# Kernel optimization log

Measured on AMD Instinct MI355X. Metric: run time of the kernel, lower is better.

## Reference

```python
import jax, jax.numpy as jnp
import numpy as np

N, E, D, H, C, ED = 100000, 1600000, 128, 8, 16, 16  # nodes, edges, dim, heads, out_ch, edge_dim
NEG_SLOPE = 0.2
LN_EPS = 1e-5


def setup_inputs() -> dict:
    key = jax.random.key(0)
    ks = jax.random.split(key, 16)
    g = 1.0 / np.sqrt(D)
    return {
        "x": jax.random.normal(ks[0], (N, D), jnp.float32),
        "edge_index": jax.random.randint(ks[1], (2, E), 0, N, dtype=jnp.int64),
        "edge_attr": jax.random.normal(ks[2], (E, ED), jnp.float32),
        "lin_W": jax.random.normal(ks[3], (D, H * C), jnp.float32) * g,
        "att_src": jax.random.normal(ks[4], (1, H, C), jnp.float32) * g,
        "att_dst": jax.random.normal(ks[5], (1, H, C), jnp.float32) * g,
        "lin_edge_W": jax.random.normal(ks[6], (ED, H * C), jnp.float32) * (1.0 / np.sqrt(ED)),
        "att_edge": jax.random.normal(ks[7], (1, H, C), jnp.float32) * g,
        "conv_bias": jnp.zeros((H * C,), jnp.float32),
        "ln1_g": jnp.ones((D,), jnp.float32),
        "ln1_b": jnp.zeros((D,), jnp.float32),
        "W1": jax.random.normal(ks[8], (D, D), jnp.float32) * g,
        "b1": jnp.zeros((D,), jnp.float32),
        "W2": jax.random.normal(ks[9], (D, D), jnp.float32) * g,
        "b2": jnp.zeros((D,), jnp.float32),
        "ln2_g": jnp.ones((D,), jnp.float32),
        "ln2_b": jnp.zeros((D,), jnp.float32),
    }


def _layernorm(v, g, b):
    mu = jnp.mean(v, axis=-1, keepdims=True)
    var = jnp.mean(jnp.square(v - mu), axis=-1, keepdims=True)
    return (v - mu) * jax.lax.rsqrt(var + LN_EPS) * g + b


def reference(x, edge_index, edge_attr, lin_W, att_src, att_dst, lin_edge_W,
              att_edge, conv_bias, ln1_g, ln1_b, W1, b1, W2, b2, ln2_g, ln2_b):
    src, dst = edge_index[0], edge_index[1]
    xh = (x @ lin_W).reshape(N, H, C)              # [N,H,C]
    a_src = jnp.sum(xh * att_src, axis=-1)         # [N,H]
    a_dst = jnp.sum(xh * att_dst, axis=-1)         # [N,H]
    e = (edge_attr @ lin_edge_W).reshape(E, H, C)  # [E,H,C]
    alpha = a_src[src] + a_dst[dst] + jnp.sum(e * att_edge, axis=-1)  # [E,H]
    alpha = jnp.where(alpha >= 0, alpha, NEG_SLOPE * alpha)
    # segment softmax over destination nodes
    m = jax.ops.segment_max(alpha, dst, num_segments=N)  # [N,H]
    m = jnp.where(jnp.isfinite(m), m, 0.0)
    ex = jnp.exp(alpha - m[dst])
    s = jax.ops.segment_sum(ex, dst, num_segments=N)     # [N,H]
    alpha = ex / (s[dst] + 1e-16)
    # message: alpha * x_j * edge_attr (TrimConv custom message)
    msg = alpha[:, :, None] * xh[src] * e                # [E,H,C]
    out = jax.ops.segment_sum(msg, dst, num_segments=N).reshape(N, H * C) + conv_bias
    h = _layernorm(x + out, ln1_g, ln1_b)
    z = jax.nn.gelu(h @ W1 + b1, approximate=False) @ W2 + b2
    return _layernorm(h + z, ln2_g, ln2_b)
```

## Files before the change

kernel.cpp:

```cpp
#include <hip/hip_runtime.h>
#include <hip/hip_bf16.h>
#include <math.h>

#define NN 100000
#define EE 1600000
#define DD 128
#define HH 8
#define CC 16
#define EDD 16
#define NBLK 98

typedef unsigned short u16;
typedef unsigned int u32;
typedef __attribute__((ext_vector_type(8))) short short8;
typedef __attribute__((ext_vector_type(4))) float f32x4;

__device__ __forceinline__ u16 f2bf(float f) {
  u32 u = __float_as_uint(f);
  u32 r = u + 0x7fff + ((u >> 16) & 1);
  return (u16)(r >> 16);
}


__global__ void k_hist(const int* __restrict__ ei, int* __restrict__ cnt) {
  int stride = gridDim.x * blockDim.x;
  for (int e = blockIdx.x * blockDim.x + threadIdx.x; e < EE; e += stride)
    atomicAdd(&cnt[ei[EE + e]], 1);
}

__global__ __launch_bounds__(1024) void k_scan_a(const int* __restrict__ cnt,
                                                 int* __restrict__ loc,
                                                 int* __restrict__ bsum) {
  __shared__ int wpart[16];
  int t = threadIdx.x, lane = t & 63, w = t >> 6;
  int i = blockIdx.x * 1024 + t;
  int v = (i < NN) ? cnt[i] : 0;
  int x = v;
#pragma unroll
  for (int d = 1; d < 64; d <<= 1) {
    int y = __shfl_up(x, d, 64);
    if (lane >= d) x += y;
  }
  if (lane == 63) wpart[w] = x;
  __syncthreads();
  if (w == 0) {
    int p = (lane < 16) ? wpart[lane] : 0;
#pragma unroll
    for (int d = 1; d < 16; d <<= 1) {
      int y = __shfl_up(p, d, 64);
      if (lane >= d) p += y;
    }
    if (lane < 16) wpart[lane] = p;
  }
  __syncthreads();
  int excl = ((w > 0) ? wpart[w - 1] : 0) + (x - v);
  if (i < NN) loc[i] = excl;
  if (t == 0) bsum[blockIdx.x] = wpart[15];
}

__global__ void k_scan_b(int* __restrict__ bsum, int* __restrict__ off) {
  if (blockIdx.x == 0 && threadIdx.x == 0) {
    int run = 0;
    for (int b = 0; b < NBLK; b++) { int s = bsum[b]; bsum[b] = run; run += s; }
    off[NN] = run;
  }
}

__global__ __launch_bounds__(1024) void k_scan_c(const int* __restrict__ loc,
                                                 const int* __restrict__ bsum,
                                                 int* __restrict__ off,
                                                 int* __restrict__ cur) {
  int i = blockIdx.x * 1024 + threadIdx.x;
  if (i < NN) {
    int v = loc[i] + bsum[i >> 10];
    off[i] = v;
    cur[i] = v;
  }
}

__global__ void k_scatter(const int* __restrict__ ei, int* __restrict__ cur,
                          int* __restrict__ perm) {
  int stride = gridDim.x * blockDim.x;
  for (int e = blockIdx.x * blockDim.x + threadIdx.x; e < EE; e += stride) {
    int d = ei[EE + e];
    int p = atomicAdd(&cur[d], 1);
    perm[p] = e;
  }
}


__global__ void k_gather(const int* __restrict__ perm, const int* __restrict__ ei,
                         const float* __restrict__ eattr, float* __restrict__ eattrP,
                         int* __restrict__ srcP) {
  int stride = gridDim.x * blockDim.x;
  for (int c = blockIdx.x * blockDim.x + threadIdx.x; c < EE * 4; c += stride) {
    int ii = c >> 2, q = c & 3;
    int e = perm[ii];
    ((float4*)eattrP)[ii * 4 + q] = ((const float4*)eattr)[e * 4 + q];
    if (q == 0) srcP[ii] = ei[e];
  }
}


__global__ void k_prep(const float* __restrict__ linW, const float* __restrict__ W1,
                       const float* __restrict__ W2, const float* __restrict__ wle,
                       const float* __restrict__ attE, u16* __restrict__ Btg,
                       float* __restrict__ WAg) {
  int tid = blockIdx.x * 256 + threadIdx.x;
  if (tid < 6144) {
    int m = tid >> 11;
    int cid = tid & 2047;
    const float* W = (m == 0) ? linW : (m == 1) ? W1 : W2;
    int n = cid >> 4, kc = cid & 15;
    union { u16 us[8]; uint4 q4; } P;
#pragma unroll
    for (int j = 0; j < 8; j++) P.us[j] = f2bf(W[(kc * 8 + j) * 128 + n]);
    ((uint4*)(Btg + (size_t)m * 16384))[cid] = P.q4;
  } else if (tid < 6272) {
    int i = tid - 6144;
    int k = i >> 3, h = i & 7;
    float s = 0.f;
#pragma unroll
    for (int c = 0; c < 16; c++) s += wle[k * 128 + h * 16 + c] * attE[h * 16 + c];
    WAg[k * 8 + h] = s;
  }
}


template <int EPI>
__global__ __launch_bounds__(256) void k_gemm(
    const float* __restrict__ A, const u16* __restrict__ Bt,
    const float* __restrict__ bias, const float* __restrict__ resid,
    const float* __restrict__ lng, const float* __restrict__ lnb,
    float* __restrict__ Cout) {
  __shared__ u16 As[64 * 136];
  __shared__ u16 Bs[128 * 136];
  int t = threadIdx.x;
  int row0 = blockIdx.x * 64;
#pragma unroll
  for (int i = 0; i < 8; i++) {
    int cid = t + 256 * i;
    int n = cid >> 4, kc = cid & 15;
    uint4 v = ((const uint4*)Bt)[cid];
    *((uint4*)(&Bs[n * 136 + kc * 8])) = v;
  }
  {
    int r = t >> 2, q = t & 3;
    const float* Ar = A + (size_t)(row0 + r) * 128 + q * 32;
    bool ok = (row0 + r) < NN;
#pragma unroll
    for (int j = 0; j < 4; j++) {
      float4 u = ok ? ((const float4*)Ar)[2 * j] : make_float4(0.f, 0.f, 0.f, 0.f);
      float4 v = ok ? ((const float4*)Ar)[2 * j + 1] : make_float4(0.f, 0.f, 0.f, 0.f);
      union { u16 us[8]; uint4 q4; } P;
      P.us[0] = f2bf(u.x); P.us[1] = f2bf(u.y); P.us[2] = f2bf(u.z); P.us[3] = f2bf(u.w);
      P.us[4] = f2bf(v.x); P.us[5] = f2bf(v.y); P.us[6] = f2bf(v.z); P.us[7] = f2bf(v.w);
      *((uint4*)(&As[r * 136 + (q * 4 + j) * 8])) = P.q4;
    }
  }
  __syncthreads();
  int w = t >> 6, lane = t & 63, lo = lane & 15, hi = lane >> 4;
  f32x4 acc[8];
  f32x4 zero = {0.f, 0.f, 0.f, 0.f};
#pragma unroll
  for (int i = 0; i < 8; i++) acc[i] = zero;
  const u16* ApL = &As[(w * 16 + lo) * 136];
  const u16* BpL = &Bs[lo * 136];
#pragma unroll
  for (int ks = 0; ks < 4; ks++) {
    short8 af = *((const short8*)(ApL + ks * 32 + hi * 8));
#pragma unroll
    for (int tt = 0; tt < 8; tt++) {
      short8 bf = *((const short8*)(BpL + tt * 16 * 136 + ks * 32 + hi * 8));
      acc[tt] = __builtin_amdgcn_mfma_f32_16x16x32_bf16(af, bf, acc[tt], 0, 0, 0);
    }
  }
  if (EPI == 0) {
#pragma unroll
    for (int j = 0; j < 4; j++) {
      int row = row0 + w * 16 + hi * 4 + j;
      if (row < NN) {
#pragma unroll
        for (int tt = 0; tt < 8; tt++)
          Cout[(size_t)row * 128 + tt * 16 + lo] = acc[tt][j];
      }
    }
  } else if (EPI == 1) {
#pragma unroll
    for (int j = 0; j < 4; j++) {
      int row = row0 + w * 16 + hi * 4 + j;
      if (row < NN) {
#pragma unroll
        for (int tt = 0; tt < 8; tt++) {
          int col = tt * 16 + lo;
          float z = acc[tt][j] + bias[col];
          float g = 0.5f * z * (1.f + erff(z * 0.70710678118654752f));
          Cout[(size_t)row * 128 + col] = g;
        }
      }
    }
  } else {
#pragma unroll
    for (int j = 0; j < 4; j++) {
      int row = row0 + w * 16 + hi * 4 + j;
      bool rok = row < NN;
      float v[8];
      float sum = 0.f;
#pragma unroll
      for (int tt = 0; tt < 8; tt++) {
        int col = tt * 16 + lo;
        float hv = rok ? resid[(size_t)row * 128 + col] : 0.f;
        v[tt] = hv + acc[tt][j] + bias[col];
        sum += v[tt];
      }
      sum += __shfl_xor(sum, 1, 64); sum += __shfl_xor(sum, 2, 64);
      sum += __shfl_xor(sum, 4, 64); sum += __shfl_xor(sum, 8, 64);
      float mu = sum * (1.f / 128.f);
      float var = 0.f;
#pragma unroll
      for (int tt = 0; tt < 8; tt++) { v[tt] -= mu; var += v[tt] * v[tt]; }
      var += __shfl_xor(var, 1, 64); var += __shfl_xor(var, 2, 64);
      var += __shfl_xor(var, 4, 64); var += __shfl_xor(var, 8, 64);
      float rs = rsqrtf(var * (1.f / 128.f) + 1e-5f);
      if (rok) {
#pragma unroll
        for (int tt = 0; tt < 8; tt++) {
          int col = tt * 16 + lo;
          Cout[(size_t)row * 128 + col] = v[tt] * rs * lng[col] + lnb[col];
        }
      }
    }
  }
}


__global__ __launch_bounds__(256) void k_att(const float* __restrict__ xh,
                                             const float* __restrict__ attS,
                                             const float* __restrict__ attD,
                                             float* __restrict__ asrc,
                                             float* __restrict__ adst) {
  int w = threadIdx.x >> 6, lane = threadIdx.x & 63;
  int n = blockIdx.x * 4 + w;
  if (n >= NN) return;
  float v0 = xh[(size_t)n * 128 + lane];
  float v1 = xh[(size_t)n * 128 + 64 + lane];
  float s0 = v0 * attS[lane], s1 = v1 * attS[64 + lane];
  float d0 = v0 * attD[lane], d1 = v1 * attD[64 + lane];
#pragma unroll
  for (int m = 1; m < 16; m <<= 1) {
    s0 += __shfl_xor(s0, m, 64); s1 += __shfl_xor(s1, m, 64);
    d0 += __shfl_xor(d0, m, 64); d1 += __shfl_xor(d1, m, 64);
  }
  if ((lane & 15) == 0) {
    int h = lane >> 4;
    asrc[n * HH + h] = s0; asrc[n * HH + 4 + h] = s1;
    adst[n * HH + h] = d0; adst[n * HH + 4 + h] = d1;
  }
}


template <bool GATHER>
__global__ __launch_bounds__(256, 4) void k_agg(
    const int* __restrict__ ei, const float* __restrict__ eattr,
    const float* __restrict__ eattrP, const int* __restrict__ srcP,
    const int* __restrict__ perm, const float* __restrict__ wle,
    const float* __restrict__ wag, const float* __restrict__ x,
    const float* __restrict__ xh, const float* __restrict__ asrc,
    const float* __restrict__ adst, const float* __restrict__ cbias,
    const float* __restrict__ ln1g, const float* __restrict__ ln1b,
    const int* __restrict__ off, float* __restrict__ hbuf) {
  int w = threadIdx.x >> 6, lane = threadIdx.x & 63;
  int n = blockIdx.x * 4 + w;
  if (n >= NN) return;
  int h = lane >> 3;
  float wlA[16], wlB[16], wa[16];
#pragma unroll
  for (int k = 0; k < 16; k++) {
    float2 tv = *(const float2*)(wle + k * 128 + 2 * lane);
    wlA[k] = tv.x; wlB[k] = tv.y;
    wa[k] = wag[k * 8 + h];
  }
  float ad = adst[n * HH + h];
  int st = off[n], cnt = off[n + 1] - st;
  float accA = 0.f, accB = 0.f, ssum = 0.f;

  const float* erows = GATHER ? eattrP : eattr;

#define SRCQ(q) ((q) < cnt ? (GATHER ? srcP[st + (q)] : ei[perm[st + (q)]]) : 0)
#define ROWQ(q) ((q) < cnt ? (GATHER ? (st + (q)) : perm[st + (q)]) : 0)

  int s0 = SRCQ(0), s1 = SRCQ(1);
  int r0 = ROWQ(0);
  const float4* p0 = (const float4*)(erows + (size_t)r0 * 16);
  float4 a0 = p0[0], a1 = p0[1], a2 = p0[2], a3 = p0[3];
  float2 xf0 = *(const float2*)(xh + (size_t)s0 * 128 + 2 * lane);
  float as0 = asrc[s0 * HH + h];
  float2 xf1 = *(const float2*)(xh + (size_t)s1 * 128 + 2 * lane);
  float as1 = asrc[s1 * HH + h];

  for (int q = 0; q < cnt; ++q) {
    int r1 = ROWQ(q + 1);
    const float4* pn = (const float4*)(erows + (size_t)r1 * 16);
    float4 b0 = pn[0], b1 = pn[1], b2 = pn[2], b3 = pn[3];
    int s2 = SRCQ(q + 2);
    float2 xf2 = *(const float2*)(xh + (size_t)s2 * 128 + 2 * lane);
    float as2 = asrc[s2 * HH + h];
    float ea[16] = {a0.x, a0.y, a0.z, a0.w, a1.x, a1.y, a1.z, a1.w,
                    a2.x, a2.y, a2.z, a2.w, a3.x, a3.y, a3.z, a3.w};
    float evA = 0.f, evB = 0.f, pe = 0.f;
#pragma unroll
    for (int k = 0; k < 16; k++) {
      evA += ea[k] * wlA[k];
      evB += ea[k] * wlB[k];
      pe += ea[k] * wa[k];
    }
    float al = as0 + ad + pe;
    al = (al >= 0.f) ? al : 0.2f * al;
    float ex = __expf(al);
    ssum += ex;
    accA += ex * xf0.x * evA;
    accB += ex * xf0.y * evB;
    a0 = b0; a1 = b1; a2 = b2; a3 = b3;
    xf0 = xf1; as0 = as1;
    xf1 = xf2; as1 = as2;
  }
#undef SRCQ
#undef ROWQ

  float inv = 1.f / (ssum + 1e-16f);
  float2 cb = *(const float2*)(cbias + 2 * lane);
  float2 xv = *(const float2*)(x + (size_t)n * 128 + 2 * lane);
  float v0 = xv.x + accA * inv + cb.x;
  float v1 = xv.y + accB * inv + cb.y;
  float sum = v0 + v1;
#pragma unroll
  for (int m = 1; m < 64; m <<= 1) sum += __shfl_xor(sum, m, 64);
  float mu = sum * (1.f / 128.f);
  float q0 = v0 - mu, q1 = v1 - mu;
  float vs = q0 * q0 + q1 * q1;
#pragma unroll
  for (int m = 1; m < 64; m <<= 1) vs += __shfl_xor(vs, m, 64);
  float rs = rsqrtf(vs * (1.f / 128.f) + 1e-5f);
  float2 g = *(const float2*)(ln1g + 2 * lane);
  float2 b = *(const float2*)(ln1b + 2 * lane);
  float2 o;
  o.x = q0 * rs * g.x + b.x;
  o.y = q1 * rs * g.y + b.y;
  *(float2*)(hbuf + (size_t)n * 128 + 2 * lane) = o;
}


#define WS_XH 0ull
#define WS_HBUF 51200000ull
#define WS_ASRC 102400000ull
#define WS_ADST 105600000ull
#define WS_OFF 108800000ull
#define WS_CUR 109200128ull
#define WS_PERM 109600128ull
#define WS_WAG 116000128ull
#define WS_BTG 116000640ull
#define WS_SRCP 116098944ull
#define WS_EATTRP 122498944ull
#define WS_NEED_GATHER 224898944ull

extern "C" void kernel_launch(void* const* d_in, const int* in_sizes, int n_in,
                              void* d_out, int out_size, void* d_ws, size_t ws_size,
                              hipStream_t stream) {
  const float* x     = (const float*)d_in[0];
  const int*   ei    = (const int*)d_in[1];
  const float* eattr = (const float*)d_in[2];
  const float* linW  = (const float*)d_in[3];
  const float* attS  = (const float*)d_in[4];
  const float* attD  = (const float*)d_in[5];
  const float* wle   = (const float*)d_in[6];
  const float* attE  = (const float*)d_in[7];
  const float* cbias = (const float*)d_in[8];
  const float* ln1g  = (const float*)d_in[9];
  const float* ln1b  = (const float*)d_in[10];
  const float* W1    = (const float*)d_in[11];
  const float* mb1   = (const float*)d_in[12];
  const float* W2    = (const float*)d_in[13];
  const float* mb2   = (const float*)d_in[14];
  const float* ln2g  = (const float*)d_in[15];
  const float* ln2b  = (const float*)d_in[16];

  char* ws = (char*)d_ws;
  float* xh     = (float*)(ws + WS_XH);
  float* hbuf   = (float*)(ws + WS_HBUF);
  float* asrc   = (float*)(ws + WS_ASRC);
  float* adst   = (float*)(ws + WS_ADST);
  int*   off    = (int*)(ws + WS_OFF);
  int*   cur    = (int*)(ws + WS_CUR);
  int*   perm   = (int*)(ws + WS_PERM);
  float* WAg    = (float*)(ws + WS_WAG);
  u16*   Btg    = (u16*)(ws + WS_BTG);
  int*   srcP   = (int*)(ws + WS_SRCP);
  float* eattrP = (float*)(ws + WS_EATTRP);
  int*   loc    = (int*)(ws + WS_XH);
  int*   bsum   = (int*)(ws + WS_ADST);
  float* outp   = (float*)d_out;

  bool gather = ws_size >= WS_NEED_GATHER;

  hipMemsetAsync(cur, 0, NN * sizeof(int), stream);
  k_hist<<<4096, 256, 0, stream>>>(ei, cur);
  k_scan_a<<<NBLK, 1024, 0, stream>>>(cur, loc, bsum);
  k_scan_b<<<1, 64, 0, stream>>>(bsum, off);
  k_scan_c<<<NBLK, 1024, 0, stream>>>(loc, bsum, off, cur);
  k_scatter<<<4096, 256, 0, stream>>>(ei, cur, perm);
  k_prep<<<25, 256, 0, stream>>>(linW, W1, W2, wle, attE, Btg, WAg);
  if (gather)
    k_gather<<<4096, 256, 0, stream>>>(perm, ei, eattr, eattrP, srcP);
  k_gemm<0><<<(NN + 63) / 64, 256, 0, stream>>>(x, Btg, x, x, x, x, xh);
  k_att<<<(NN + 3) / 4, 256, 0, stream>>>(xh, attS, attD, asrc, adst);
  if (gather)
    k_agg<true><<<(NN + 3) / 4, 256, 0, stream>>>(
        ei, eattr, eattrP, srcP, perm, wle, WAg, x, xh, asrc, adst, cbias,
        ln1g, ln1b, off, hbuf);
  else
    k_agg<false><<<(NN + 3) / 4, 256, 0, stream>>>(
        ei, eattr, eattrP, srcP, perm, wle, WAg, x, xh, asrc, adst, cbias,
        ln1g, ln1b, off, hbuf);
  k_gemm<1><<<(NN + 63) / 64, 256, 0, stream>>>(hbuf, Btg + 16384, mb1, hbuf,
                                                ln2g, ln2b, xh);
  k_gemm<2><<<(NN + 63) / 64, 256, 0, stream>>>(xh, Btg + 32768, mb2, hbuf,
                                                ln2g, ln2b, outp);
}
```

Measured before the change: 1.019 ms.

## Split aggregation into edge-parallel message kernel and bf16 node reduce

Stores the node projection xh in bf16 and adds an edge-parallel kernel. That kernel computes per-edge bf16 messages and attention logits in destination-sorted order. A lighter per-node kernel then does the softmax reduction and LayerNorm. This aims to balance the edge work and halve the random gather bytes, at the cost of writing and re-reading a large message buffer and of reduced bf16 precision. The separate eattr gather pass is removed, and the MLP intermediate now reuses the output buffer.

New measurement: 1.238 ms. 21.4% more time.

```diff
diff --git a/kernel.cpp b/kernel.cpp
--- a/kernel.cpp
+++ b/kernel.cpp
@@ -85,19 +85,6 @@
     int d = ei[EE + e];
     int p = atomicAdd(&cur[d], 1);
     perm[p] = e;
-  }
-}
-
-
-__global__ void k_gather(const int* __restrict__ perm, const int* __restrict__ ei,
-                         const float* __restrict__ eattr, float* __restrict__ eattrP,
-                         int* __restrict__ srcP) {
-  int stride = gridDim.x * blockDim.x;
-  for (int c = blockIdx.x * blockDim.x + threadIdx.x; c < EE * 4; c += stride) {
-    int ii = c >> 2, q = c & 3;
-    int e = perm[ii];
-    ((float4*)eattrP)[ii * 4 + q] = ((const float4*)eattr)[e * 4 + q];
-    if (q == 0) srcP[ii] = ei[e];
   }
 }
 
@@ -185,6 +172,17 @@
           Cout[(size_t)row * 128 + tt * 16 + lo] = acc[tt][j];
       }
     }
+  } else if (EPI == 3) {
+    u16* Cb = (u16*)Cout;
+#pragma unroll
+    for (int j = 0; j < 4; j++) {
+      int row = row0 + w * 16 + hi * 4 + j;
+      if (row < NN) {
+#pragma unroll
+        for (int tt = 0; tt < 8; tt++)
+          Cb[(size_t)row * 128 + tt * 16 + lo] = f2bf(acc[tt][j]);
+      }
+    }
   } else if (EPI == 1) {
 #pragma unroll
     for (int j = 0; j < 4; j++) {
@@ -234,11 +232,35 @@
 }
 
 
-__global__ __launch_bounds__(256) void k_att(const float* __restrict__ xh,
-                                             const float* __restrict__ attS,
-                                             const float* __restrict__ attD,
-                                             float* __restrict__ asrc,
-                                             float* __restrict__ adst) {
+__global__ __launch_bounds__(256) void k_att_b(const u16* __restrict__ xhb,
+                                               const float* __restrict__ attS,
+                                               const float* __restrict__ attD,
+                                               float* __restrict__ asrc,
+                                               float* __restrict__ adst) {
+  int w = threadIdx.x >> 6, lane = threadIdx.x & 63;
+  int n = blockIdx.x * 4 + w;
+  if (n >= NN) return;
+  u32 xp = ((const u32*)xhb)[(size_t)n * 64 + lane];
+  float x0 = __uint_as_float(xp << 16);
+  float x1 = __uint_as_float(xp & 0xffff0000u);
+  float2 as = *(const float2*)(attS + 2 * lane);
+  float2 ad = *(const float2*)(attD + 2 * lane);
+  float s = x0 * as.x + x1 * as.y;
+  float d = x0 * ad.x + x1 * ad.y;
+  s += __shfl_xor(s, 1, 64); s += __shfl_xor(s, 2, 64); s += __shfl_xor(s, 4, 64);
+  d += __shfl_xor(d, 1, 64); d += __shfl_xor(d, 2, 64); d += __shfl_xor(d, 4, 64);
+  if ((lane & 7) == 0) {
+    int h = lane >> 3;
+    asrc[n * HH + h] = s;
+    adst[n * HH + h] = d;
+  }
+}
+
+__global__ __launch_bounds__(256) void k_att_f(const float* __restrict__ xh,
+                                               const float* __restrict__ attS,
+                                               const float* __restrict__ attD,
+                                               float* __restrict__ asrc,
+                                               float* __restrict__ adst) {
   int w = threadIdx.x >> 6, lane = threadIdx.x & 63;
   int n = blockIdx.x * 4 + w;
   if (n >= NN) return;
@@ -259,10 +281,100 @@
 }
 
 
-template <bool GATHER>
-__global__ __launch_bounds__(256, 4) void k_agg(
+__global__ __launch_bounds__(256) void k_edge(
+    const int* __restrict__ ei, const int* __restrict__ perm,
+    const float* __restrict__ eattr, const float* __restrict__ wle,
+    const float* __restrict__ wag, const u16* __restrict__ xhb,
+    const float* __restrict__ asrc, u16* __restrict__ mP,
+    float* __restrict__ lgv) {
+  int lane = threadIdx.x & 63;
+  int wid = (blockIdx.x * blockDim.x + threadIdx.x) >> 6;
+  int nw = (gridDim.x * blockDim.x) >> 6;
+  int h = lane >> 3;
+  float wlA[16], wlB[16], wa[16];
+#pragma unroll
+  for (int k = 0; k < 16; k++) {
+    float2 tv = *(const float2*)(wle + k * 128 + 2 * lane);
+    wlA[k] = tv.x; wlB[k] = tv.y;
+    wa[k] = wag[k * 8 + h];
+  }
+  for (int ii = wid; ii < EE; ii += nw) {
+    int e = perm[ii];
+    int src = ei[e];
+    const float4* eap = (const float4*)(eattr + (size_t)e * EDD);
+    float4 a0 = eap[0], a1 = eap[1], a2 = eap[2], a3 = eap[3];
+    u32 xp = ((const u32*)xhb)[(size_t)src * 64 + lane];
+    float ea[16] = {a0.x, a0.y, a0.z, a0.w, a1.x, a1.y, a1.z, a1.w,
+                    a2.x, a2.y, a2.z, a2.w, a3.x, a3.y, a3.z, a3.w};
+    float evA = 0.f, evB = 0.f, pe = 0.f;
+#pragma unroll
+    for (int k = 0; k < 16; k++) {
+      evA += ea[k] * wlA[k];
+      evB += ea[k] * wlB[k];
+      pe += ea[k] * wa[k];
+    }
+    float x0 = __uint_as_float(xp << 16);
+    float x1 = __uint_as_float(xp & 0xffff0000u);
+    u32 mpk = (u32)f2bf(x0 * evA) | ((u32)f2bf(x1 * evB) << 16);
+    ((u32*)mP)[(size_t)ii * 64 + lane] = mpk;
+    if ((lane & 7) == 0) lgv[(size_t)ii * 8 + h] = asrc[src * HH + h] + pe;
+  }
+}
+
+
+__global__ __launch_bounds__(256, 4) void k_agg2(
+    const u16* __restrict__ mP, const float* __restrict__ lgv,
+    const float* __restrict__ adst, const float* __restrict__ x,
+    const float* __restrict__ cbias, const float* __restrict__ ln1g,
+    const float* __restrict__ ln1b, const int* __restrict__ off,
+    float* __restrict__ hbuf) {
+  int w = threadIdx.x >> 6, lane = threadIdx.x & 63;
+  int n = blockIdx.x * 4 + w;
+  if (n >= NN) return;
+  int h = lane >> 3;
+  float ad = adst[n * HH + h];
+  int st = off[n], cnt = off[n + 1] - st;
+  const u32* mp = (const u32*)mP + (size_t)st * 64 + lane;
+  const float* lp = lgv + (size_t)st * 8 + h;
+  float accA = 0.f, accB = 0.f, ssum = 0.f;
+  u32 m_c = 0; float lg_c = 0.f;
+  if (cnt > 0) { m_c = mp[0]; lg_c = lp[0]; }
+  for (int q = 0; q < cnt; ++q) {
+    u32 m_n = 0; float lg_n = 0.f;
+    if (q + 1 < cnt) { m_n = mp[(size_t)(q + 1) * 64]; lg_n = lp[(size_t)(q + 1) * 8]; }
+    float al = lg_c + ad;
+    al = (al >= 0.f) ? al : 0.2f * al;
+    float ex = __expf(al);
+    ssum += ex;
+    accA += ex * __uint_as_float(m_c << 16);
+    accB += ex * __uint_as_float(m_c & 0xffff0000u);
+    m_c = m_n; lg_c = lg_n;
+  }
+  float inv = 1.f / (ssum + 1e-16f);
+  float2 cb = *(const float2*)(cbias + 2 * lane);
+  float2 xv = *(const float2*)(x + (size_t)n * 128 + 2 * lane);
+  float v0 = xv.x + accA * inv + cb.x;
+  float v1 = xv.y + accB * inv + cb.y;
+  float sum = v0 + v1;
+#pragma unroll
+  for (int m = 1; m < 64; m <<= 1) sum += __shfl_xor(sum, m, 64);
+  float mu = sum * (1.f / 128.f);
+  float q0 = v0 - mu, q1 = v1 - mu;
+  float vs = q0 * q0 + q1 * q1;
+#pragma unroll
+  for (int m = 1; m < 64; m <<= 1) vs += __shfl_xor(vs, m, 64);
+  float rs = rsqrtf(vs * (1.f / 128.f) + 1e-5f);
+  float2 g = *(const float2*)(ln1g + 2 * lane);
+  float2 b = *(const float2*)(ln1b + 2 * lane);
+  float2 o;
+  o.x = q0 * rs * g.x + b.x;
+  o.y = q1 * rs * g.y + b.y;
+  *(float2*)(hbuf + (size_t)n * 128 + 2 * lane) = o;
+}
+
+
+__global__ __launch_bounds__(256, 4) void k_agg_lite(
     const int* __restrict__ ei, const float* __restrict__ eattr,
-    const float* __restrict__ eattrP, const int* __restrict__ srcP,
     const int* __restrict__ perm, const float* __restrict__ wle,
     const float* __restrict__ wag, const float* __restrict__ x,
     const float* __restrict__ xh, const float* __restrict__ asrc,
@@ -283,24 +395,19 @@
   float ad = adst[n * HH + h];
   int st = off[n], cnt = off[n + 1] - st;
   float accA = 0.f, accB = 0.f, ssum = 0.f;
-
-  const float* erows = GATHER ? eattrP : eattr;
-
-#define SRCQ(q) ((q) < cnt ? (GATHER ? srcP[st + (q)] : ei[perm[st + (q)]]) : 0)
-#define ROWQ(q) ((q) < cnt ? (GATHER ? (st + (q)) : perm[st + (q)]) : 0)
-
+#define SRCQ(q) ((q) < cnt ? ei[perm[st + (q)]] : 0)
+#define ROWQ(q) ((q) < cnt ? perm[st + (q)] : 0)
   int s0 = SRCQ(0), s1 = SRCQ(1);
   int r0 = ROWQ(0);
-  const float4* p0 = (const float4*)(erows + (size_t)r0 * 16);
+  const float4* p0 = (const float4*)(eattr + (size_t)r0 * EDD);
   float4 a0 = p0[0], a1 = p0[1], a2 = p0[2], a3 = p0[3];
   float2 xf0 = *(const float2*)(xh + (size_t)s0 * 128 + 2 * lane);
   float as0 = asrc[s0 * HH + h];
   float2 xf1 = *(const float2*)(xh + (size_t)s1 * 128 + 2 * lane);
   float as1 = asrc[s1 * HH + h];
-
   for (int q = 0; q < cnt; ++q) {
     int r1 = ROWQ(q + 1);
-    const float4* pn = (const float4*)(erows + (size_t)r1 * 16);
+    const float4* pn = (const float4*)(eattr + (size_t)r1 * EDD);
     float4 b0 = pn[0], b1 = pn[1], b2 = pn[2], b3 = pn[3];
     int s2 = SRCQ(q + 2);
     float2 xf2 = *(const float2*)(xh + (size_t)s2 * 128 + 2 * lane);
@@ -326,7 +433,6 @@
   }
 #undef SRCQ
 #undef ROWQ
-
   float inv = 1.f / (ssum + 1e-16f);
   float2 cb = *(const float2*)(cbias + 2 * lane);
   float2 xv = *(const float2*)(x + (size_t)n * 128 + 2 * lane);
@@ -350,18 +456,27 @@
 }
 
 
-#define WS_XH 0ull
-#define WS_HBUF 51200000ull
-#define WS_ASRC 102400000ull
-#define WS_ADST 105600000ull
-#define WS_OFF 108800000ull
-#define WS_CUR 109200128ull
-#define WS_PERM 109600128ull
-#define WS_WAG 116000128ull
-#define WS_BTG 116000640ull
-#define WS_SRCP 116098944ull
-#define WS_EATTRP 122498944ull
-#define WS_NEED_GATHER 224898944ull
+#define WF_MP 0ull
+#define WF_LG 409600000ull
+#define WF_HBUF 460800000ull
+#define WF_XHB 512000000ull
+#define WF_ASRC 537600000ull
+#define WF_ADST 540800000ull
+#define WF_OFF 544000000ull
+#define WF_CUR 544400128ull
+#define WF_PERM 544800256ull
+#define WF_BTG 551200256ull
+#define WF_WAG 551298560ull
+#define WF_NEED 551302656ull
+#define WL_XH 0ull
+#define WL_HBUF 51200000ull
+#define WL_ASRC 102400000ull
+#define WL_ADST 105600000ull
+#define WL_OFF 108800000ull
+#define WL_CUR 109200128ull
+#define WL_PERM 109600128ull
+#define WL_WAG 116000128ull
+#define WL_BTG 116000640ull
 
 extern "C" void kernel_launch(void* const* d_in, const int* in_sizes, int n_in,
                               void* d_out, int out_size, void* d_ws, size_t ws_size,
@@ -385,44 +500,68 @@
   const float* ln2b  = (const float*)d_in[16];
 
   char* ws = (char*)d_ws;
-  float* xh     = (float*)(ws + WS_XH);
-  float* hbuf   = (float*)(ws + WS_HBUF);
-  float* asrc   = (float*)(ws + WS_ASRC);
-  float* adst   = (float*)(ws + WS_ADST);
-  int*   off    = (int*)(ws + WS_OFF);
-  int*   cur    = (int*)(ws + WS_CUR);
-  int*   perm   = (int*)(ws + WS_PERM);
-  float* WAg    = (float*)(ws + WS_WAG);
-  u16*   Btg    = (u16*)(ws + WS_BTG);
-  int*   srcP   = (int*)(ws + WS_SRCP);
-  float* eattrP = (float*)(ws + WS_EATTRP);
-  int*   loc    = (int*)(ws + WS_XH);
-  int*   bsum   = (int*)(ws + WS_ADST);
-  float* outp   = (float*)d_out;
-
-  bool gather = ws_size >= WS_NEED_GATHER;
-
-  hipMemsetAsync(cur, 0, NN * sizeof(int), stream);
-  k_hist<<<4096, 256, 0, stream>>>(ei, cur);
-  k_scan_a<<<NBLK, 1024, 0, stream>>>(cur, loc, bsum);
-  k_scan_b<<<1, 64, 0, stream>>>(bsum, off);
-  k_scan_c<<<NBLK, 1024, 0, stream>>>(loc, bsum, off, cur);
-  k_scatter<<<4096, 256, 0, stream>>>(ei, cur, perm);
-  k_prep<<<25, 256, 0, stream>>>(linW, W1, W2, wle, attE, Btg, WAg);
-  if (gather)
-    k_gather<<<4096, 256, 0, stream>>>(perm, ei, eattr, eattrP, srcP);
-  k_gemm<0><<<(NN + 63) / 64, 256, 0, stream>>>(x, Btg, x, x, x, x, xh);
-  k_att<<<(NN + 3) / 4, 256, 0, stream>>>(xh, attS, attD, asrc, adst);
-  if (gather)
-    k_agg<true><<<(NN + 3) / 4, 256, 0, stream>>>(
-        ei, eattr, eattrP, srcP, perm, wle, WAg, x, xh, asrc, adst, cbias,
-        ln1g, ln1b, off, hbuf);
-  else
-    k_agg<false><<<(NN + 3) / 4, 256, 0, stream>>>(
-        ei, eattr, eattrP, srcP, perm, wle, WAg, x, xh, asrc, adst, cbias,
-        ln1g, ln1b, off, hbuf);
-  k_gemm<1><<<(NN + 63) / 64, 256, 0, stream>>>(hbuf, Btg + 16384, mb1, hbuf,
-                                                ln2g, ln2b, xh);
-  k_gemm<2><<<(NN + 63) / 64, 256, 0, stream>>>(xh, Btg + 32768, mb2, hbuf,
-                                                ln2g, ln2b, outp);
-}
+  float* outp = (float*)d_out;
+  bool full = ws_size >= WF_NEED;
+
+  if (full) {
+    u16*   mP   = (u16*)(ws + WF_MP);
+    float* lgv  = (float*)(ws + WF_LG);
+    float* hbuf = (float*)(ws + WF_HBUF);
+    u16*   xhb  = (u16*)(ws + WF_XHB);
+    float* asrc = (float*)(ws + WF_ASRC);
+    float* adst = (float*)(ws + WF_ADST);
+    int*   off  = (int*)(ws + WF_OFF);
+    int*   cur  = (int*)(ws + WF_CUR);
+    int*   perm = (int*)(ws + WF_PERM);
+    u16*   Btg  = (u16*)(ws + WF_BTG);
+    float* WAg  = (float*)(ws + WF_WAG);
+    int*   loc  = (int*)(ws + WF_MP);
+    int*   bsum = (int*)(ws + WF_LG);
+
+    hipMemsetAsync(cur, 0, NN * sizeof(int), stream);
+    k_hist<<<4096, 256, 0, stream>>>(ei, cur);
+    k_scan_a<<<NBLK, 1024, 0, stream>>>(cur, loc, bsum);
+    k_scan_b<<<1, 64, 0, stream>>>(bsum, off);
+    k_scan_c<<<NBLK, 1024, 0, stream>>>(loc, bsum, off, cur);
+    k_scatter<<<4096, 256, 0, stream>>>(ei, cur, perm);
+    k_prep<<<25, 256, 0, stream>>>(linW, W1, W2, wle, attE, Btg, WAg);
+    k_gemm<3><<<(NN + 63) / 64, 256, 0, stream>>>(x, Btg, x, x, x, x, (float*)xhb);
+    k_att_b<<<(NN + 3) / 4, 256, 0, stream>>>(xhb, attS, attD, asrc, adst);
+    k_edge<<<2048, 256, 0, stream>>>(ei, perm, eattr, wle, WAg, xhb, asrc, mP, lgv);
+    k_agg2<<<(NN + 3) / 4, 256, 0, stream>>>(mP, lgv, adst, x, cbias, ln1g, ln1b,
+                                             off, hbuf);
+    k_gemm<1><<<(NN + 63) / 64, 256, 0, stream>>>(hbuf, Btg + 16384, mb1, hbuf,
+                                                  ln2g, ln2b, outp);
+    k_gemm<2><<<(NN + 63) / 64, 256, 0, stream>>>(outp, Btg + 32768, mb2, hbuf,
+                                                  ln2g, ln2b, outp);
+  } else {
+    float* xh   = (float*)(ws + WL_XH);
+    float* hbuf = (float*)(ws + WL_HBUF);
+    float* asrc = (float*)(ws + WL_ASRC);
+    float* adst = (float*)(ws + WL_ADST);
+    int*   off  = (int*)(ws + WL_OFF);
+    int*   cur  = (int*)(ws + WL_CUR);
+    int*   perm = (int*)(ws + WL_PERM);
+    float* WAg  = (float*)(ws + WL_WAG);
+    u16*   Btg  = (u16*)(ws + WL_BTG);
+    int*   loc  = (int*)(ws + WL_XH);
+    int*   bsum = (int*)(ws + WL_ADST);
+
+    hipMemsetAsync(cur, 0, NN * sizeof(int), stream);
+    k_hist<<<4096, 256, 0, stream>>>(ei, cur);
+    k_scan_a<<<NBLK, 1024, 0, stream>>>(cur, loc, bsum);
+    k_scan_b<<<1, 64, 0, stream>>>(bsum, off);
+    k_scan_c<<<NBLK, 1024, 0, stream>>>(loc, bsum, off, cur);
+    k_scatter<<<4096, 256, 0, stream>>>(ei, cur, perm);
+    k_prep<<<25, 256, 0, stream>>>(linW, W1, W2, wle, attE, Btg, WAg);
+    k_gemm<0><<<(NN + 63) / 64, 256, 0, stream>>>(x, Btg, x, x, x, x, xh);
+    k_att_f<<<(NN + 3) / 4, 256, 0, stream>>>(xh, attS, attD, asrc, adst);
+    k_agg_lite<<<(NN + 3) / 4, 256, 0, stream>>>(ei, eattr, perm, wle, WAg, x, xh,
+                                                 asrc, adst, cbias, ln1g, ln1b,
+                                                 off, hbuf);
+    k_gemm<1><<<(NN + 63) / 64, 256, 0, stream>>>(hbuf, Btg + 16384, mb1, hbuf,
+                                                  ln2g, ln2b, xh);
+    k_gemm<2><<<(NN + 63) / 64, 256, 0, stream>>>(xh, Btg + 32768, mb2, hbuf,
+                                                  ln2g, ln2b, outp);
+  }
+}
```
